# Performance work log

Hardware: AMD Instinct MI355X
Metric: run time of the kernel (lower is better)

The kernel has to match this reference:

```python
import jax, jax.numpy as jnp
import numpy as np

NUM_GROUPS = 32
EPS = 1e-6


def group_norm(x, gamma, beta):
    # x: [b, c, h, w]
    b, c, h, w = x.shape
    xg = x.reshape(b, NUM_GROUPS, c // NUM_GROUPS, h, w)
    mean = jnp.mean(xg, axis=(2, 3, 4), keepdims=True)
    var = jnp.var(xg, axis=(2, 3, 4), keepdims=True)
    xn = ((xg - mean) * jax.lax.rsqrt(var + EPS)).reshape(b, c, h, w)
    return xn * gamma[None, :, None, None] + beta[None, :, None, None]


def setup_inputs() -> dict:
    key = jax.random.key(0)
    ks = jax.random.split(key, 8)
    B, C, H, W = 4, 512, 64, 64
    s = 0.02  # small init so softmax is well-conditioned
    return {
        "x": jax.random.normal(ks[0], (B, C, H, W), dtype=jnp.float32),
        "gamma": jnp.ones((C,), dtype=jnp.float32),
        "beta": jnp.zeros((C,), dtype=jnp.float32),
        "wq": jax.random.normal(ks[1], (C, C), dtype=jnp.float32) * s,
        "bq": jnp.zeros((C,), dtype=jnp.float32),
        "wk": jax.random.normal(ks[2], (C, C), dtype=jnp.float32) * s,
        "bk": jnp.zeros((C,), dtype=jnp.float32),
        "wv": jax.random.normal(ks[3], (C, C), dtype=jnp.float32) * s,
        "bv": jnp.zeros((C,), dtype=jnp.float32),
        "wp": jax.random.normal(ks[4], (C, C), dtype=jnp.float32) * s,
        "bp": jnp.zeros((C,), dtype=jnp.float32),
    }


def reference(x, gamma, beta, wq, bq, wk, bk, wv, bv, wp, bp):
    b, c, h, w = x.shape
    hw = h * w
    h_ = group_norm(x, gamma, beta).reshape(b, c, hw)  # [b, c, hw]
    # 1x1 convs == channel matmuls
    q = jnp.einsum('oc,bcn->bon', wq, h_) + bq[None, :, None]
    k = jnp.einsum('oc,bcn->bon', wk, h_) + bk[None, :, None]
    v = jnp.einsum('oc,bcn->bon', wv, h_) + bv[None, :, None]
    # scores[b, n, m] = sum_c q[b,c,n] k[b,c,m]
    scores = jnp.einsum('bcn,bcm->bnm', q, k) * (c ** -0.5)
    attn = jax.nn.softmax(scores, axis=2)  # over keys m
    # out[b, c, n] = sum_m v[b,c,m] * attn[b,n,m]
    o = jnp.einsum('bcm,bnm->bcn', v, attn)
    o = jnp.einsum('oc,bcn->bon', wp, o) + bp[None, :, None]
    return x + o.reshape(b, c, h, w)
```

## Files before the change

### kernel.cpp

```cpp
#include <hip/hip_runtime.h>
#include <hip/hip_bf16.h>

constexpr int BATCH = 4;
constexpr int CH    = 512;
constexpr int HWN   = 4096;
constexpr int NG    = 32;
constexpr float SM_SCALE = 0.044194173824159216f;
constexpr float SM_L2E   = 0.06376608440f;

__device__ __align__(256) ushort g_ht[(long)BATCH*HWN*CH];
__device__ __align__(256) ushort g_qt[(long)BATCH*HWN*CH];
__device__ __align__(256) ushort g_kt[(long)BATCH*HWN*CH];
__device__ __align__(256) ushort g_v [(long)BATCH*CH*HWN];
__device__ __align__(256) ushort g_S [(long)BATCH*HWN*HWN];
__device__ __align__(256) ushort g_ot[(long)BATCH*HWN*CH];
__device__ __align__(256) ushort g_wq[CH*CH], g_wk[CH*CH], g_wv[CH*CH], g_wp[CH*CH];
__device__ float g_mean[BATCH*NG], g_rstd[BATCH*NG];
__device__ float g_rowsum[BATCH*HWN];

typedef short v8s __attribute__((ext_vector_type(8)));
typedef float f32x4 __attribute__((ext_vector_type(4)));

__device__ inline ushort f2b(float f){
  __hip_bfloat16 h = __float2bfloat16(f);
  return __builtin_bit_cast(ushort, h);
}

__device__ inline void gload16(const ushort* g, ushort* lds_base){
  __builtin_amdgcn_global_load_lds(
      (const __attribute__((address_space(1))) unsigned int*)g,
      (__attribute__((address_space(3))) unsigned int*)lds_base, 16, 0, 0);
}

__device__ inline void blockbar(){
  asm volatile("" ::: "memory");
  __builtin_amdgcn_s_barrier();
  asm volatile("" ::: "memory");
}

__global__ __launch_bounds__(256) void prep_weights(const float* wq, const float* wk,
                                                    const float* wv, const float* wp){
  int t = blockIdx.x*256 + threadIdx.x;
  g_wq[t] = f2b(wq[t]);
  g_wk[t] = f2b(wk[t]);
  g_wv[t] = f2b(wv[t]);
  g_wp[t] = f2b(wp[t]);
  if (t < BATCH*HWN) g_rowsum[t] = 0.0f;
}

__global__ __launch_bounds__(256) void gn_stats(const float* x){
  __shared__ float ss[4], ss2[4];
  const float4* p = (const float4*)(x + (long)blockIdx.x*65536);
  float s = 0.f, s2 = 0.f;
  for (int i = threadIdx.x; i < 16384; i += 256){
    float4 v = p[i];
    s  += v.x + v.y + v.z + v.w;
    s2 += v.x*v.x + v.y*v.y + v.z*v.z + v.w*v.w;
  }
  for (int off = 1; off < 64; off <<= 1){
    s  += __shfl_xor(s,  off);
    s2 += __shfl_xor(s2, off);
  }
  if ((threadIdx.x & 63) == 0){ ss[threadIdx.x>>6] = s; ss2[threadIdx.x>>6] = s2; }
  __syncthreads();
  if (threadIdx.x == 0){
    float S1 = ss[0]+ss[1]+ss[2]+ss[3], S2 = ss2[0]+ss2[1]+ss2[2]+ss2[3];
    float mean = S1 * (1.0f/65536.0f);
    float var  = S2 * (1.0f/65536.0f) - mean*mean;
    g_mean[blockIdx.x] = mean;
    g_rstd[blockIdx.x] = rsqrtf(var + 1e-6f);
  }
}

__global__ __launch_bounds__(256) void gn_apply(const float* x, const float* gamma, const float* beta){
  __shared__ ushort tile[64][72];
  const int b = blockIdx.z, tc = blockIdx.y, tn = blockIdx.x;
  const int t = threadIdx.x;
  const int r = t >> 4;
  const int ncol = (t & 15) * 4;
  const float* xb = x + ((long)b*CH + tc*64)*HWN + tn*64;
  #pragma unroll
  for (int rg = 0; rg < 4; rg++){
    int c_local = rg*16 + r;
    int c = tc*64 + c_local;
    int gidx = b*NG + (c >> 4);
    float mean = g_mean[gidx], rstd = g_rstd[gidx];
    float ga = gamma[c], be = beta[c];
    float4 v = *(const float4*)(xb + (long)c_local*HWN + ncol);
    tile[c_local][ncol+0] = f2b((v.x - mean)*rstd*ga + be);
    tile[c_local][ncol+1] = f2b((v.y - mean)*rstd*ga + be);
    tile[c_local][ncol+2] = f2b((v.z - mean)*rstd*ga + be);
    tile[c_local][ncol+3] = f2b((v.w - mean)*rstd*ga + be);
  }
  __syncthreads();
  ushort* ht = g_ht + ((long)b*HWN + tn*64)*CH + tc*64;
  #pragma unroll
  for (int rg = 0; rg < 4; rg++){
    int n_local = rg*16 + r;
    int cl = (t & 15) * 4;
    ushort4 pk;
    pk.x = tile[cl+0][n_local];
    pk.y = tile[cl+1][n_local];
    pk.z = tile[cl+2][n_local];
    pk.w = tile[cl+3][n_local];
    *(ushort4*)(ht + (long)n_local*CH + cl) = pk;
  }
}

template<int CFG>
__global__ __launch_bounds__(256, 2) void gemm_bt(const float* bias, const float* xres, float* outf){
  constexpr int Kdim = CH;
  constexpr int BIAS = (CFG==0 || CFG==1) ? 2 : (CFG==2) ? 1 : 0;

  __shared__ __align__(16) ushort As[128*32];
  __shared__ __align__(16) ushort Bs[128*32];

  const int z = blockIdx.z;
  const int tm = blockIdx.x, tn = blockIdx.y;
  const int t = threadIdx.x;

  const ushort *Ap, *Bp;  ushort* Cp = nullptr;
  int lda, ldb, ldc = 0;
  if constexpr (CFG==0){ Ap=g_ht+(long)z*HWN*CH; Bp=g_wq; Cp=g_qt+(long)z*HWN*CH; lda=CH;  ldb=CH;  ldc=CH;  }
  if constexpr (CFG==1){ Ap=g_ht+(long)z*HWN*CH; Bp=g_wk; Cp=g_kt+(long)z*HWN*CH; lda=CH;  ldb=CH;  ldc=CH;  }
  if constexpr (CFG==2){ Ap=g_wv; Bp=g_ht+(long)z*HWN*CH; Cp=g_v +(long)z*CH*HWN; lda=CH;  ldb=CH;  ldc=HWN; }
  if constexpr (CFG==5){ Ap=g_ot+(long)z*HWN*CH; Bp=g_wp; lda=CH; ldb=CH; }

  const int lane = t & 63, wid = t >> 6;
  const int wr = (wid >> 1) * 64, wc = (wid & 1) * 64;
  const int lr = lane & 15, lk = lane >> 4;

  const int srow = t >> 2, sko = t & 3;
  const int wave_base = (t & 192) * 8;

  f32x4 acc[4][4] = {};

  for (int kt = 0; kt < Kdim; kt += 32){
    __syncthreads();
    #pragma unroll
    for (int i = 0; i < 2; i++){
      int row = srow + i*64;
      const ushort* ga = Ap + (long)(tm*128 + row)*lda + kt + sko*8;
      const ushort* gb = Bp + (long)(tn*128 + row)*ldb + kt + sko*8;
      gload16(ga, As + wave_base + i*256*8);
      gload16(gb, Bs + wave_base + i*256*8);
    }
    __syncthreads();
    v8s af[4], bfr[4];
    #pragma unroll
    for (int mi = 0; mi < 4; mi++){
      int row = wr + mi*16 + lr;
      af[mi] = *(const v8s*)(As + row*32 + lk*8);
    }
    #pragma unroll
    for (int ni = 0; ni < 4; ni++){
      int row = wc + ni*16 + lr;
      bfr[ni] = *(const v8s*)(Bs + row*32 + lk*8);
    }
    #pragma unroll
    for (int mi = 0; mi < 4; mi++)
      #pragma unroll
      for (int ni = 0; ni < 4; ni++)
        acc[mi][ni] = __builtin_amdgcn_mfma_f32_16x16x32_bf16(af[mi], bfr[ni], acc[mi][ni], 0, 0, 0);
  }

  if constexpr (CFG==5){
    float* ob = outf + (long)z*CH*HWN;
    const float* xb = xres + (long)z*CH*HWN;
    #pragma unroll
    for (int mi = 0; mi < 4; mi++){
      #pragma unroll
      for (int ni = 0; ni < 4; ni++){
        int col = tn*128 + wc + ni*16 + lr;
        int rowm = tm*128 + wr + mi*16 + lk*4;
        float cb = bias[col];
        long off = (long)col*HWN + rowm;
        float4 xv = *(const float4*)(xb + off);
        float4 ov;
        ov.x = acc[mi][ni][0] + cb + xv.x;
        ov.y = acc[mi][ni][1] + cb + xv.y;
        ov.z = acc[mi][ni][2] + cb + xv.z;
        ov.w = acc[mi][ni][3] + cb + xv.w;
        *(float4*)(ob + off) = ov;
      }
    }
  } else {
    #pragma unroll
    for (int mi = 0; mi < 4; mi++){
      #pragma unroll
      for (int ni = 0; ni < 4; ni++){
        int col = tn*128 + wc + ni*16 + lr;
        float cb = 0.f;
        if constexpr (BIAS==2) cb = bias[col];
        #pragma unroll
        for (int j = 0; j < 4; j++){
          int rowm = tm*128 + wr + mi*16 + lk*4 + j;
          float v = acc[mi][ni][j];
          if constexpr (BIAS==1) v += bias[rowm]; else v += cb;
          Cp[(long)rowm*ldc + col] = f2b(v);
        }
      }
    }
  }
}

template<int CFG>
__global__ __launch_bounds__(512, 2) void gemm256(){
  constexpr int Kdim = (CFG==4) ? HWN : CH;
  constexpr int BN   = (CFG==3) ? 256 : 128;
  constexpr int NI   = BN/64;
  constexpr int NI2  = NI/2;
  constexpr int AUNITS = 2048;
  constexpr int BUNITS = BN*64/8;
  constexpr int BH   = BUNITS/2;
  constexpr int BBIT = (CFG==3) ? 5 : 4;
  constexpr int Lb   = BH/512;
  constexpr int DBUF = AUNITS + BUNITS;
  constexpr int NT = Kdim/64, NITER = NT/2;

  __shared__ __align__(16) ushort lds[DBUF*2*8];

  const int t = threadIdx.x, lane = t & 63, wid = t >> 6;
  const int wm = wid >> 2, wn = wid & 3;
  const int lr = lane & 15, lk = lane >> 4;
  const int tm = blockIdx.x, tn = blockIdx.y, z = blockIdx.z;

  const ushort *Ap, *Bp; ushort* Cp; long lda, ldb, ldc;
  if constexpr (CFG==3){
    Ap = g_qt + (long)z*HWN*CH; lda = CH;
    Bp = g_kt + (long)z*HWN*CH; ldb = CH;
    Cp = g_S  + (long)z*HWN*HWN; ldc = HWN;
  } else {
    Ap = g_S  + (long)z*HWN*HWN; lda = HWN;
    Bp = g_v  + (long)z*CH*HWN;  ldb = HWN;
    Cp = g_ot + (long)z*HWN*CH;  ldc = CH;
  }

  const int srw  = lane >> 3;
  const int sc16 = (lane & 7) ^ srw;
  const int rxor = lr & 7;

  auto stageA = [&](int h, int T){
    #pragma unroll
    for (int j = 0; j < 2; j++){
      int W = wid*2 + j;
      int RH = W*8 + srw;
      int r = (RH>>6)*128 + h*64 + (RH&63);
      gload16(Ap + (long)(tm*256 + r)*lda + T*64 + sc16*8,
              lds + ((T&1)*DBUF + h*1024 + W*64)*8);
    }
  };
  auto stageB = [&](int h, int T){
    #pragma unroll
    for (int j = 0; j < Lb; j++){
      int W = wid*Lb + j;
      int RH = W*8 + srw;
      int r = (RH>>BBIT)*(2<<BBIT) + h*(1<<BBIT) + (RH & ((1<<BBIT)-1));
      gload16(Bp + (long)(tn*BN + r)*ldb + T*64 + sc16*8,
              lds + ((T&1)*DBUF + AUNITS + h*BH + W*64)*8);
    }
  };
  auto readA = [&](int d, int h, v8s (&a)[4][2]){
    #pragma unroll
    for (int mp = 0; mp < 4; mp++){
      int RH = wm*64 + mp*16 + lr;
      #pragma unroll
      for (int kk = 0; kk < 2; kk++){
        int u = d*DBUF + h*1024 + RH*8 + ((kk*4 + lk) ^ rxor);
        a[mp][kk] = *(const v8s*)(lds + u*8);
      }
    }
  };
  auto readB = [&](int d, int h, v8s (&b)[NI2][2]){
    #pragma unroll
    for (int np = 0; np < NI2; np++){
      int RH = (CFG==3) ? (wn*32 + np*16 + lr) : (wn*16 + lr);
      #pragma unroll
      for (int kk = 0; kk < 2; kk++){
        int u = d*DBUF + AUNITS + h*BH + RH*8 + ((kk*4 + lk) ^ rxor);
        b[np][kk] = *(const v8s*)(lds + u*8);
      }
    }
  };

  f32x4 acc[8][NI] = {};
  auto mm = [&](const v8s (&a)[4][2], const v8s (&b)[NI2][2], int mh, int nh){
    __builtin_amdgcn_s_setprio(1);
    #pragma unroll
    for (int mp = 0; mp < 4; mp++)
      #pragma unroll
      for (int np = 0; np < NI2; np++)
        #pragma unroll
        for (int kk = 0; kk < 2; kk++)
          acc[mh*4+mp][nh*NI2+np] = __builtin_amdgcn_mfma_f32_16x16x32_bf16(
              a[mp][kk], b[np][kk], acc[mh*4+mp][nh*NI2+np], 0, 0, 0);
    __builtin_amdgcn_s_setprio(0);
  };

  #define VM_STEADY() do { if constexpr (CFG==3) asm volatile("s_waitcnt vmcnt(4)" ::: "memory"); \
                           else                  asm volatile("s_waitcnt vmcnt(3)" ::: "memory"); } while(0)
  #define VM_DRAIN()  asm volatile("s_waitcnt vmcnt(0)" ::: "memory")

  stageA(0, 0); stageB(0, 0); stageA(1, 0); stageB(1, 0); stageA(0, 1); stageB(0, 1);
  VM_STEADY();
  blockbar();

  for (int it = 0; it < NITER; ++it){
    const int X = 2*it, Y = X + 1;
    const bool last = (it == NITER-1);
    v8s a[4][2], b[NI2][2];

    stageA(1, Y);
    readA(0, 0, a); readB(0, 0, b);
    mm(a, b, 0, 0);
    blockbar();
    stageB(1, Y);
    readA(0, 1, a);
    mm(a, b, 1, 0);
    blockbar();
    if (!last) stageB(0, X+2);
    readB(0, 1, b); readA(0, 0, a);
    mm(a, b, 0, 1);
    blockbar();
    if (!last) stageA(0, X+2);
    readA(0, 1, a);
    mm(a, b, 1, 1);
    if (last) VM_DRAIN(); else VM_STEADY();
    blockbar();
    if (!last) stageA(1, X+2);
    readA(1, 0, a); readB(1, 0, b);
    mm(a, b, 0, 0);
    blockbar();
    if (!last) stageB(1, X+2);
    readA(1, 1, a);
    mm(a, b, 1, 0);
    blockbar();
    if (!last) stageB(0, Y+2);
    readB(1, 1, b); readA(1, 0, a);
    mm(a, b, 0, 1);
    blockbar();
    if (!last) stageA(0, Y+2);
    readA(1, 1, a);
    mm(a, b, 1, 1);
    if (!last) VM_STEADY();
    blockbar();
  }
  #undef VM_STEADY
  #undef VM_DRAIN

  if constexpr (CFG==3){
    float rs[8][4] = {};
    #pragma unroll
    for (int mi = 0; mi < 8; mi++){
      #pragma unroll
      for (int ni = 0; ni < NI; ni++){
        int col = tn*256 + wn*64 + ni*16 + lr;
        #pragma unroll
        for (int j = 0; j < 4; j++){
          float p = exp2f(acc[mi][ni][j] * SM_L2E);
          int row = tm*256 + wm*128 + mi*16 + lk*4 + j;
          Cp[(long)row*ldc + col] = f2b(p);
          rs[mi][j] += p;
        }
      }
    }
    float* rsum = g_rowsum + (long)z*HWN;
    #pragma unroll
    for (int mi = 0; mi < 8; mi++){
      #pragma unroll
      for (int j = 0; j < 4; j++){
        float s = rs[mi][j];
        s += __shfl_xor(s, 1); s += __shfl_xor(s, 2);
        s += __shfl_xor(s, 4); s += __shfl_xor(s, 8);
        if (lr == 0)
          atomicAdd(&rsum[tm*256 + wm*128 + mi*16 + lk*4 + j], s);
      }
    }
  } else {
    const float* rsum = g_rowsum + (long)z*HWN;
    #pragma unroll
    for (int mi = 0; mi < 8; mi++){
      int rowb = tm*256 + wm*128 + mi*16 + lk*4;
      float4 s4 = *(const float4*)(rsum + rowb);
      float inv[4] = {1.0f/s4.x, 1.0f/s4.y, 1.0f/s4.z, 1.0f/s4.w};
      #pragma unroll
      for (int ni = 0; ni < NI; ni++){
        int col = tn*BN + wn*32 + ni*16 + lr;
        #pragma unroll
        for (int j = 0; j < 4; j++)
          Cp[(long)(rowb + j)*ldc + col] = f2b(acc[mi][ni][j] * inv[j]);
      }
    }
  }
}

extern "C" void kernel_launch(void* const* d_in, const int* in_sizes, int n_in,
                              void* d_out, int out_size, void* d_ws, size_t ws_size,
                              hipStream_t stream){
  const float* x     = (const float*)d_in[0];
  const float* gamma = (const float*)d_in[1];
  const float* beta  = (const float*)d_in[2];
  const float* wq    = (const float*)d_in[3];
  const float* bq    = (const float*)d_in[4];
  const float* wk    = (const float*)d_in[5];
  const float* bk    = (const float*)d_in[6];
  const float* wv    = (const float*)d_in[7];
  const float* bv    = (const float*)d_in[8];
  const float* wp    = (const float*)d_in[9];
  const float* bp    = (const float*)d_in[10];
  float* out = (float*)d_out;

  prep_weights<<<1024, 256, 0, stream>>>(wq, wk, wv, wp);
  gn_stats<<<BATCH*NG, 256, 0, stream>>>(x);
  gn_apply<<<dim3(HWN/64, CH/64, BATCH), 256, 0, stream>>>(x, gamma, beta);

  gemm_bt<0><<<dim3(HWN/128, CH/128, BATCH), 256, 0, stream>>>(bq, nullptr, nullptr);
  gemm_bt<1><<<dim3(HWN/128, CH/128, BATCH), 256, 0, stream>>>(bk, nullptr, nullptr);
  gemm_bt<2><<<dim3(CH/128, HWN/128, BATCH), 256, 0, stream>>>(bv, nullptr, nullptr);
  gemm256<3><<<dim3(HWN/256, HWN/256, BATCH), 512, 0, stream>>>();
  gemm256<4><<<dim3(HWN/256, CH/128, BATCH), 512, 0, stream>>>();
  gemm_bt<5><<<dim3(HWN/128, CH/128, BATCH), 256, 0, stream>>>(bp, x, out);
}
```

Before: 419.7 us.

## Fuse Q/K projections into one GEMM and move scores GEMM to 128-tile kernel

```diff
diff --git a/kernel.cpp b/kernel.cpp
--- a/kernel.cpp
+++ b/kernel.cpp
@@ -9,12 +9,13 @@
 constexpr float SM_L2E   = 0.06376608440f;
 
 __device__ __align__(256) ushort g_ht[(long)BATCH*HWN*CH];
-__device__ __align__(256) ushort g_qt[(long)BATCH*HWN*CH];
-__device__ __align__(256) ushort g_kt[(long)BATCH*HWN*CH];
+__device__ __align__(256) ushort g_qk[(long)BATCH*HWN*1024];
 __device__ __align__(256) ushort g_v [(long)BATCH*CH*HWN];
 __device__ __align__(256) ushort g_S [(long)BATCH*HWN*HWN];
 __device__ __align__(256) ushort g_ot[(long)BATCH*HWN*CH];
-__device__ __align__(256) ushort g_wq[CH*CH], g_wk[CH*CH], g_wv[CH*CH], g_wp[CH*CH];
+__device__ __align__(256) ushort g_wqk[2*CH*CH];
+__device__ __align__(256) ushort g_wv[CH*CH], g_wp[CH*CH];
+__device__ float g_bqk[2*CH];
 __device__ float g_mean[BATCH*NG], g_rstd[BATCH*NG];
 __device__ float g_rowsum[BATCH*HWN];
 
@@ -39,13 +40,15 @@
 }
 
 __global__ __launch_bounds__(256) void prep_weights(const float* wq, const float* wk,
-                                                    const float* wv, const float* wp){
+                                                    const float* wv, const float* wp,
+                                                    const float* bq, const float* bk){
   int t = blockIdx.x*256 + threadIdx.x;
-  g_wq[t] = f2b(wq[t]);
-  g_wk[t] = f2b(wk[t]);
+  g_wqk[t]        = f2b(wq[t]);
+  g_wqk[CH*CH+t]  = f2b(wk[t]);
   g_wv[t] = f2b(wv[t]);
   g_wp[t] = f2b(wp[t]);
   if (t < BATCH*HWN) g_rowsum[t] = 0.0f;
+  if (t < 2*CH) g_bqk[t] = (t < CH) ? bq[t] : bk[t-CH];
 }
 
 __global__ __launch_bounds__(256) void gn_stats(const float* x){
@@ -110,7 +113,6 @@
 template<int CFG>
 __global__ __launch_bounds__(256, 2) void gemm_bt(const float* bias, const float* xres, float* outf){
   constexpr int Kdim = CH;
-  constexpr int BIAS = (CFG==0 || CFG==1) ? 2 : (CFG==2) ? 1 : 0;
 
   __shared__ __align__(16) ushort As[128*32];
   __shared__ __align__(16) ushort Bs[128*32];
@@ -120,10 +122,10 @@
   const int t = threadIdx.x;
 
   const ushort *Ap, *Bp;  ushort* Cp = nullptr;
-  int lda, ldb, ldc = 0;
-  if constexpr (CFG==0){ Ap=g_ht+(long)z*HWN*CH; Bp=g_wq; Cp=g_qt+(long)z*HWN*CH; lda=CH;  ldb=CH;  ldc=CH;  }
-  if constexpr (CFG==1){ Ap=g_ht+(long)z*HWN*CH; Bp=g_wk; Cp=g_kt+(long)z*HWN*CH; lda=CH;  ldb=CH;  ldc=CH;  }
-  if constexpr (CFG==2){ Ap=g_wv; Bp=g_ht+(long)z*HWN*CH; Cp=g_v +(long)z*CH*HWN; lda=CH;  ldb=CH;  ldc=HWN; }
+  long lda, ldb, ldc = 0;
+  if constexpr (CFG==0){ Ap=g_ht+(long)z*HWN*CH; Bp=g_wqk; Cp=g_qk+(long)z*HWN*1024; lda=CH; ldb=CH; ldc=1024; }
+  if constexpr (CFG==2){ Ap=g_wv; Bp=g_ht+(long)z*HWN*CH; Cp=g_v +(long)z*CH*HWN; lda=CH; ldb=CH; ldc=HWN; }
+  if constexpr (CFG==3){ Ap=g_qk+(long)z*HWN*1024; Bp=Ap+512; Cp=g_S+(long)z*HWN*HWN; lda=1024; ldb=1024; ldc=HWN; }
   if constexpr (CFG==5){ Ap=g_ot+(long)z*HWN*CH; Bp=g_wp; lda=CH; ldb=CH; }
 
   const int lane = t & 63, wid = t >> 6;
@@ -164,7 +166,40 @@
         acc[mi][ni] = __builtin_amdgcn_mfma_f32_16x16x32_bf16(af[mi], bfr[ni], acc[mi][ni], 0, 0, 0);
   }
 
-  if constexpr (CFG==5){
+  if constexpr (CFG==3){
+    float rs[4][4] = {};
+    #pragma unroll
+    for (int mi = 0; mi < 4; mi++){
+      #pragma unroll
+      for (int ni = 0; ni < 4; ni++){
+        int col = tn*128 + wc + ni*16 + lr;
+        #pragma unroll
+        for (int j = 0; j < 4; j++){
+          float p = exp2f(acc[mi][ni][j] * SM_L2E);
+          int rowm = tm*128 + wr + mi*16 + lk*4 + j;
+          Cp[(long)rowm*ldc + col] = f2b(p);
+          rs[mi][j] += p;
+        }
+      }
+    }
+    #pragma unroll
+    for (int mi = 0; mi < 4; mi++)
+      #pragma unroll
+      for (int j = 0; j < 4; j++){
+        float s = rs[mi][j];
+        s += __shfl_xor(s, 1); s += __shfl_xor(s, 2);
+        s += __shfl_xor(s, 4); s += __shfl_xor(s, 8);
+        rs[mi][j] = s;
+      }
+    if (lr == 0){
+      float* rsum = g_rowsum + (long)z*HWN;
+      #pragma unroll
+      for (int mi = 0; mi < 4; mi++)
+        #pragma unroll
+        for (int j = 0; j < 4; j++)
+          atomicAdd(&rsum[tm*128 + wr + mi*16 + lk*4 + j], rs[mi][j]);
+    }
+  } else if constexpr (CFG==5){
     float* ob = outf + (long)z*CH*HWN;
     const float* xb = xres + (long)z*CH*HWN;
     #pragma unroll
@@ -191,12 +226,12 @@
       for (int ni = 0; ni < 4; ni++){
         int col = tn*128 + wc + ni*16 + lr;
         float cb = 0.f;
-        if constexpr (BIAS==2) cb = bias[col];
+        if constexpr (CFG==0) cb = g_bqk[col];
         #pragma unroll
         for (int j = 0; j < 4; j++){
           int rowm = tm*128 + wr + mi*16 + lk*4 + j;
           float v = acc[mi][ni][j];
-          if constexpr (BIAS==1) v += bias[rowm]; else v += cb;
+          if constexpr (CFG==2) v += bias[rowm]; else v += cb;
           Cp[(long)rowm*ldc + col] = f2b(v);
         }
       }
@@ -226,11 +261,7 @@
   const int tm = blockIdx.x, tn = blockIdx.y, z = blockIdx.z;
 
   const ushort *Ap, *Bp; ushort* Cp; long lda, ldb, ldc;
-  if constexpr (CFG==3){
-    Ap = g_qt + (long)z*HWN*CH; lda = CH;
-    Bp = g_kt + (long)z*HWN*CH; ldb = CH;
-    Cp = g_S  + (long)z*HWN*HWN; ldc = HWN;
-  } else {
+  {
     Ap = g_S  + (long)z*HWN*HWN; lda = HWN;
     Bp = g_v  + (long)z*CH*HWN;  ldb = HWN;
     Cp = g_ot + (long)z*HWN*CH;  ldc = CH;
@@ -297,8 +328,7 @@
     __builtin_amdgcn_s_setprio(0);
   };
 
-  #define VM_STEADY() do { if constexpr (CFG==3) asm volatile("s_waitcnt vmcnt(4)" ::: "memory"); \
-                           else                  asm volatile("s_waitcnt vmcnt(3)" ::: "memory"); } while(0)
+  #define VM_STEADY() asm volatile("s_waitcnt vmcnt(3)" ::: "memory")
   #define VM_DRAIN()  asm volatile("s_waitcnt vmcnt(0)" ::: "memory")
 
   stageA(0, 0); stageB(0, 0); stageA(1, 0); stageB(1, 0); stageA(0, 1); stageB(0, 1);
@@ -348,35 +378,7 @@
   #undef VM_STEADY
   #undef VM_DRAIN
 
-  if constexpr (CFG==3){
-    float rs[8][4] = {};
-    #pragma unroll
-    for (int mi = 0; mi < 8; mi++){
-      #pragma unroll
-      for (int ni = 0; ni < NI; ni++){
-        int col = tn*256 + wn*64 + ni*16 + lr;
-        #pragma unroll
-        for (int j = 0; j < 4; j++){
-          float p = exp2f(acc[mi][ni][j] * SM_L2E);
-          int row = tm*256 + wm*128 + mi*16 + lk*4 + j;
-          Cp[(long)row*ldc + col] = f2b(p);
-          rs[mi][j] += p;
-        }
-      }
-    }
-    float* rsum = g_rowsum + (long)z*HWN;
-    #pragma unroll
-    for (int mi = 0; mi < 8; mi++){
-      #pragma unroll
-      for (int j = 0; j < 4; j++){
-        float s = rs[mi][j];
-        s += __shfl_xor(s, 1); s += __shfl_xor(s, 2);
-        s += __shfl_xor(s, 4); s += __shfl_xor(s, 8);
-        if (lr == 0)
-          atomicAdd(&rsum[tm*256 + wm*128 + mi*16 + lk*4 + j], s);
-      }
-    }
-  } else {
+  {
     const float* rsum = g_rowsum + (long)z*HWN;
     #pragma unroll
     for (int mi = 0; mi < 8; mi++){
@@ -410,14 +412,13 @@
   const float* bp    = (const float*)d_in[10];
   float* out = (float*)d_out;
 
-  prep_weights<<<1024, 256, 0, stream>>>(wq, wk, wv, wp);
+  prep_weights<<<1024, 256, 0, stream>>>(wq, wk, wv, wp, bq, bk);
   gn_stats<<<BATCH*NG, 256, 0, stream>>>(x);
   gn_apply<<<dim3(HWN/64, CH/64, BATCH), 256, 0, stream>>>(x, gamma, beta);
 
-  gemm_bt<0><<<dim3(HWN/128, CH/128, BATCH), 256, 0, stream>>>(bq, nullptr, nullptr);
-  gemm_bt<1><<<dim3(HWN/128, CH/128, BATCH), 256, 0, stream>>>(bk, nullptr, nullptr);
+  gemm_bt<0><<<dim3(HWN/128, 1024/128, BATCH), 256, 0, stream>>>(nullptr, nullptr, nullptr);
   gemm_bt<2><<<dim3(CH/128, HWN/128, BATCH), 256, 0, stream>>>(bv, nullptr, nullptr);
-  gemm256<3><<<dim3(HWN/256, HWN/256, BATCH), 512, 0, stream>>>();
+  gemm_bt<3><<<dim3(HWN/128, HWN/128, BATCH), 256, 0, stream>>>(nullptr, nullptr, nullptr);
   gemm256<4><<<dim3(HWN/256, CH/128, BATCH), 512, 0, stream>>>();
   gemm_bt<5><<<dim3(HWN/128, CH/128, BATCH), 256, 0, stream>>>(bp, x, out);
 }
```

After: 378.8 us. 9.7% less time.
